# Kernel optimization log

Measured on AMD Instinct MI355X. Metric: run time of the kernel, lower is better.

The kernel has to match this reference:

```python
import jax, jax.numpy as jnp
import numpy as np

N_NODES = 20000
N_EDGES = 200000
D = 64            # node_encoding
H = 4             # num_heads
GRAPH_LAYERS = 2
FLOW_ITERS = 10


def seg_softmax(logits, seg, n):
    # numerically stable softmax over segments (per-row softmax of sparse matrix)
    m = jax.ops.segment_max(logits, seg, num_segments=n)
    e = jnp.exp(logits - m[seg])
    s = jax.ops.segment_sum(e, seg, num_segments=n)
    return e / s[seg]


def setup_inputs() -> dict:
    key = jax.random.key(0)
    ks = jax.random.split(key, 12)
    sc = 1.0 / np.sqrt(D)
    return {
        "node_embeddings": jax.random.normal(ks[0], (N_NODES, D), jnp.float32),
        "demands": jax.random.normal(ks[1], (N_NODES, 1), jnp.float32),
        "edge_row": jax.random.randint(ks[2], (N_EDGES,), 0, N_NODES, jnp.int32),
        "edge_col": jax.random.randint(ks[3], (N_EDGES,), 0, N_NODES, jnp.int32),
        "W_gat": jax.random.normal(ks[4], (H, D, D), jnp.float32) * sc,
        "a_src": jax.random.normal(ks[5], (H, D), jnp.float32) * sc,
        "a_dst": jax.random.normal(ks[6], (H, D), jnp.float32) * sc,
        "Wx": jax.random.normal(ks[7], (D, 3 * D), jnp.float32) * sc,
        "Wh": jax.random.normal(ks[8], (D, 3 * D), jnp.float32) * sc,
        "b_gru": jnp.zeros((3 * D,), jnp.float32),
        "Wd": jax.random.normal(ks[9], (D + 1, 1), jnp.float32) * sc,
        "bd": jnp.zeros((1,), jnp.float32),
    }


def reference(node_embeddings, demands, edge_row, edge_col,
              W_gat, a_src, a_dst, Wx, Wh, b_gru, Wd, bd):
    n = node_embeddings.shape[0]
    h = node_embeddings

    for _ in range(GRAPH_LAYERS):
        # ---- SparseGAT over adjacency edge list ----
        f = jnp.einsum('nd,hde->hne', h, W_gat)          # [H,N,D] per-head features
        s_src = jnp.einsum('hne,he->hn', f, a_src)       # [H,N]
        s_dst = jnp.einsum('hne,he->hn', f, a_dst)       # [H,N]
        logits = jax.nn.leaky_relu(s_src[:, edge_row] + s_dst[:, edge_col], 0.2)  # [H,E]
        alpha = jax.vmap(lambda l: seg_softmax(l, edge_row, n))(logits)           # [H,E]
        msgs = alpha[:, :, None] * f[:, edge_col, :]                              # [H,E,D]
        agg = jax.vmap(lambda m: jax.ops.segment_sum(m, edge_row, num_segments=n))(msgs)  # [H,N,D]
        gat_out = agg.mean(axis=0)                       # average heads -> [N,D]

        # ---- GRU node update (relu candidate activation), state = h ----
        xg = gat_out @ Wx + b_gru                        # [N,3D]
        z = jax.nn.sigmoid(xg[:, :D] + h @ Wh[:, :D])
        r = jax.nn.sigmoid(xg[:, D:2 * D] + h @ Wh[:, D:2 * D])
        hh = jax.nn.relu(xg[:, 2 * D:] + (r * h) @ Wh[:, 2 * D:])
        h = z * h + (1.0 - z) * hh

    # ---- decoder: linear over concat(encoding, demands) ----
    pred_w = jnp.concatenate([h, demands], axis=1) @ Wd + bd   # [N,1]

    # ---- sparse softmax of (adj * pred_weights) per source row ----
    w = seg_softmax(pred_w[edge_row, 0], edge_row, n)          # [E]

    # ---- iterative sparse MCF flow solve ----
    d_pos = jax.nn.relu(demands[:, 0])                         # source injections

    def step(flow, _):
        inflow = d_pos + jax.ops.segment_sum(flow, edge_col, num_segments=n)
        return w * inflow[edge_row], None

    flow, _ = jax.lax.scan(step, jnp.zeros_like(w), None, length=FLOW_ITERS)
    return flow
```

## Files before the change

### kernel.cpp

```cpp
#include <hip/hip_runtime.h>


#define N_NODES 20000
#define N_EDGES 200000
#define FLOW_ITERS 10
#define NBLK 128
#define NTHR 512
#define NTOT (NBLK * NTHR)
#define EPT ((N_EDGES + NTOT - 1) / NTOT)
#define NPB 157
#define CAP 24
#define SLOTS NTOT
#define OFL_MAX 4096
#define NP1 (N_NODES + 1)

__device__ __forceinline__ float ld_coh(const float* p) {
    return __hip_atomic_load(p, __ATOMIC_RELAXED, __HIP_MEMORY_SCOPE_AGENT);
}
__device__ __forceinline__ int ld_coh_i(const int* p) {
    return __hip_atomic_load(p, __ATOMIC_RELAXED, __HIP_MEMORY_SCOPE_AGENT);
}
__device__ __forceinline__ void st_coh(float* p, float v) {
    __hip_atomic_store(p, v, __ATOMIC_RELAXED, __HIP_MEMORY_SCOPE_AGENT);
}
__device__ __forceinline__ void st_coh_i(int* p, int v) {
    __hip_atomic_store(p, v, __ATOMIC_RELAXED, __HIP_MEMORY_SCOPE_AGENT);
}

__device__ __forceinline__ void gbar(int* cnt, int target) {
    __syncthreads();
    if (threadIdx.x == 0) {
        __hip_atomic_fetch_add(cnt, 1, __ATOMIC_RELAXED, __HIP_MEMORY_SCOPE_AGENT);
        while (__hip_atomic_load(cnt, __ATOMIC_RELAXED, __HIP_MEMORY_SCOPE_AGENT) < target)
            __builtin_amdgcn_s_sleep(2);
    }
    __syncthreads();
}

__global__ __launch_bounds__(NTHR)
void mcf_fused(const float* __restrict__ demands,
               const int* __restrict__ edge_row,
               const int* __restrict__ edge_col,
               float* __restrict__ out,
               int* __restrict__ deg,
               int* __restrict__ fill,
               float* __restrict__ V0,
               float* __restrict__ V1b,
               int* __restrict__ pcsc,
               int* __restrict__ ofl_cnt,
               int* __restrict__ ofl_v,
               int* __restrict__ ofl_row,
               int* __restrict__ barcnt)
{
    const int tid = blockIdx.x * NTHR + threadIdx.x;
    int bar = 0;

    int rowr[EPT];
    #pragma unroll
    for (int i = 0; i < EPT; ++i) {
        int e = tid + i * NTOT;
        rowr[i] = N_NODES;
        if (e < N_EDGES) {
            int r = edge_row[e], c = edge_col[e];
            rowr[i] = r;
            __hip_atomic_fetch_add(&deg[r], 1, __ATOMIC_RELAXED, __HIP_MEMORY_SCOPE_AGENT);
            int idx = __hip_atomic_fetch_add(&fill[c], 1,
                                             __ATOMIC_RELAXED, __HIP_MEMORY_SCOPE_AGENT);
            int slot = (c / NPB) * NTHR + (c % NPB);
            if (idx < CAP) {
                st_coh_i(&pcsc[slot * CAP + idx], r);
            } else {
                int o = __hip_atomic_fetch_add(ofl_cnt, 1,
                                               __ATOMIC_RELAXED, __HIP_MEMORY_SCOPE_AGENT);
                if (o < OFL_MAX) { st_coh_i(&ofl_v[o], c); st_coh_i(&ofl_row[o], r); }
            }
        }
    }
    gbar(barcnt, NBLK * (++bar));

    const int tx = threadIdx.x;
    const int v  = blockIdx.x * NPB + tx;
    const bool active = (tx < NPB) && (v < N_NODES);
    float dposv = 0.0f, invd = 0.0f;
    int   cnt = 0, ocnt = 0;
    int   er[CAP];
    if (active) {
        dposv  = fmaxf(demands[v], 0.0f);
        int dv = ld_coh_i(&deg[v]);
        invd   = (dv > 0) ? (1.0f / (float)dv) : 0.0f;
        cnt    = min(ld_coh_i(&fill[v]), CAP);
        ocnt   = ld_coh_i(ofl_cnt);
        const int slot = blockIdx.x * NTHR + tx;
        #pragma unroll
        for (int k = 0; k < CAP; ++k) {
            int r = pcsc[slot * CAP + k];
            er[k] = (k < cnt) ? r : N_NODES;
        }
        st_coh(&V0[v], dposv * invd);
    }
    gbar(barcnt, NBLK * (++bar));

    #pragma unroll 1
    for (int j = 2; j <= FLOW_ITERS; ++j) {
        const float* Vp = (j & 1) ? V1b : V0;
        float*       Vn = (j & 1) ? V0 : V1b;
        if (active) {
            float sk[CAP];
            #pragma unroll
            for (int s = 0; s < CAP; ++s) sk[s] = ld_coh(&Vp[er[s]]);
            float acc = dposv;
            #pragma unroll
            for (int s = 0; s < CAP; ++s) acc += sk[s];
            if (ocnt > 0) {
                for (int o = 0; o < ocnt && o < OFL_MAX; ++o)
                    if (ld_coh_i(&ofl_v[o]) == v)
                        acc += ld_coh(&Vp[ld_coh_i(&ofl_row[o])]);
            }
            st_coh(&Vn[v], acc * invd);
        }
        gbar(barcnt, NBLK * (++bar));
    }

    #pragma unroll
    for (int i = 0; i < EPT; ++i) {
        int e = tid + i * NTOT;
        if (e < N_EDGES) out[e] = ld_coh(&V1b[rowr[i]]);
    }
}

extern "C" void kernel_launch(void* const* d_in, const int* in_sizes, int n_in,
                              void* d_out, int out_size, void* d_ws, size_t ws_size,
                              hipStream_t stream) {
    const float* demands  = (const float*)d_in[1];
    const int*   edge_row = (const int*)d_in[2];
    const int*   edge_col = (const int*)d_in[3];
    float*       out      = (float*)d_out;

    char* ws = (char*)d_ws;
    auto take = [&](size_t bytes) {
        void* p = (void*)ws;
        ws += (bytes + 127) & ~size_t(127);
        return p;
    };
    char* zone0 = ws;
    int*   deg     = (int*)  take(N_NODES * 4);
    int*   fill    = (int*)  take(N_NODES * 4);
    float* V0      = (float*)take(NP1 * 4);
    float* V1b     = (float*)take(NP1 * 4);
    int*   ofl_cnt = (int*)  take(4);
    int*   barcnt  = (int*)  take(4);
    size_t zone0_bytes = (size_t)(ws - zone0);
    int*   pcsc    = (int*)  take((size_t)SLOTS * CAP * 4);
    int*   ofl_v   = (int*)  take(OFL_MAX * 4);
    int*   ofl_row = (int*)  take(OFL_MAX * 4);

    hipMemsetAsync(zone0, 0x00, zone0_bytes, stream);
    mcf_fused<<<NBLK, NTHR, 0, stream>>>(demands, edge_row, edge_col, out,
                                         deg, fill, V0, V1b, pcsc,
                                         ofl_cnt, ofl_v, ofl_row, barcnt);
}
```

Before: 140.6 us.

## Build CSC via per-block LDS histograms and transposed prefix instead of global atomics

Replaces the global atomic degree and fill counters with per-block shared-memory histograms over a contiguous edge chunk. The histograms are written as packed 16-bit counts into per-block tables, and each node then reduces them to a degree and an exclusive prefix of in-edge counts per block. Edges are scattered into the fixed-capacity CSC slots using that prefix plus their local index. This removes heavy contended global atomics, but adds an extra grid barrier, 20000-int LDS zeroing and scanning per block, and 128-way strided reads per node.

```diff
diff --git a/kernel.cpp b/kernel.cpp
--- a/kernel.cpp
+++ b/kernel.cpp
@@ -6,11 +6,13 @@
 #define FLOW_ITERS 10
 #define NBLK 128
 #define NTHR 512
-#define NTOT (NBLK * NTHR)
-#define EPT ((N_EDGES + NTOT - 1) / NTOT)
+#define EPB 1563
+#define EPT ((EPB + NTHR - 1) / NTHR)
 #define NPB 157
 #define CAP 24
-#define SLOTS NTOT
+#define SLOTS (NBLK * NTHR)
+#define NWORD (N_NODES / 2)
+#define NPADV 20224
 #define OFL_MAX 4096
 #define NP1 (N_NODES + 1)
 
@@ -24,6 +26,9 @@
     __hip_atomic_store(p, v, __ATOMIC_RELAXED, __HIP_MEMORY_SCOPE_AGENT);
 }
 __device__ __forceinline__ void st_coh_i(int* p, int v) {
+    __hip_atomic_store(p, v, __ATOMIC_RELAXED, __HIP_MEMORY_SCOPE_AGENT);
+}
+__device__ __forceinline__ void st_coh_u(unsigned* p, unsigned v) {
     __hip_atomic_store(p, v, __ATOMIC_RELAXED, __HIP_MEMORY_SCOPE_AGENT);
 }
 
@@ -35,6 +40,10 @@
             __builtin_amdgcn_s_sleep(2);
     }
     __syncthreads();
+}
+
+__device__ __forceinline__ int half16(int w, int hi) {
+    return hi ? ((w >> 16) & 0xFFFF) : (w & 0xFFFF);
 }
 
 __global__ __launch_bounds__(NTHR)
@@ -42,8 +51,9 @@
                const int* __restrict__ edge_row,
                const int* __restrict__ edge_col,
                float* __restrict__ out,
-               int* __restrict__ deg,
-               int* __restrict__ fill,
+               int* __restrict__ degT,
+               int* __restrict__ inhT,
+               unsigned* __restrict__ pre32,
                float* __restrict__ V0,
                float* __restrict__ V1b,
                int* __restrict__ pcsc,
@@ -52,53 +62,116 @@
                int* __restrict__ ofl_row,
                int* __restrict__ barcnt)
 {
-    const int tid = blockIdx.x * NTHR + threadIdx.x;
+    const int tx = threadIdx.x, bx = blockIdx.x;
     int bar = 0;
 
-    int rowr[EPT];
+    __shared__ int ldsH[N_NODES];
+
+    int rowr[EPT], colr[EPT], lidx[EPT];
+    for (int i = tx; i < N_NODES; i += NTHR) ldsH[i] = 0;
+    __syncthreads();
     #pragma unroll
     for (int i = 0; i < EPT; ++i) {
-        int e = tid + i * NTOT;
-        rowr[i] = N_NODES;
-        if (e < N_EDGES) {
-            int r = edge_row[e], c = edge_col[e];
-            rowr[i] = r;
-            __hip_atomic_fetch_add(&deg[r], 1, __ATOMIC_RELAXED, __HIP_MEMORY_SCOPE_AGENT);
-            int idx = __hip_atomic_fetch_add(&fill[c], 1,
-                                             __ATOMIC_RELAXED, __HIP_MEMORY_SCOPE_AGENT);
-            int slot = (c / NPB) * NTHR + (c % NPB);
-            if (idx < CAP) {
-                st_coh_i(&pcsc[slot * CAP + idx], r);
-            } else {
-                int o = __hip_atomic_fetch_add(ofl_cnt, 1,
-                                               __ATOMIC_RELAXED, __HIP_MEMORY_SCOPE_AGENT);
-                if (o < OFL_MAX) { st_coh_i(&ofl_v[o], c); st_coh_i(&ofl_row[o], r); }
-            }
-        }
-    }
+        int local = i * NTHR + tx, e = bx * EPB + local;
+        rowr[i] = -1;
+        if (local < EPB && e < N_EDGES) {
+            rowr[i] = edge_row[e];
+            colr[i] = edge_col[e];
+            atomicAdd(&ldsH[rowr[i]], 1);
+        }
+    }
+    __syncthreads();
+    for (int wi = tx; wi < NWORD; wi += NTHR)
+        st_coh_i(&degT[bx * NWORD + wi], ldsH[2 * wi] | (ldsH[2 * wi + 1] << 16));
+    __syncthreads();
+
+    for (int i = tx; i < N_NODES; i += NTHR) ldsH[i] = 0;
+    __syncthreads();
+    #pragma unroll
+    for (int i = 0; i < EPT; ++i)
+        if (rowr[i] >= 0) lidx[i] = atomicAdd(&ldsH[colr[i]], 1);
+    __syncthreads();
+    for (int wi = tx; wi < NWORD; wi += NTHR)
+        st_coh_i(&inhT[bx * NWORD + wi], ldsH[2 * wi] | (ldsH[2 * wi + 1] << 16));
     gbar(barcnt, NBLK * (++bar));
 
-    const int tx = threadIdx.x;
-    const int v  = blockIdx.x * NPB + tx;
+    const int v = bx * NPB + tx;
     const bool active = (tx < NPB) && (v < N_NODES);
     float dposv = 0.0f, invd = 0.0f;
     int   cnt = 0, ocnt = 0;
     int   er[CAP];
     if (active) {
-        dposv  = fmaxf(demands[v], 0.0f);
-        int dv = ld_coh_i(&deg[v]);
-        invd   = (dv > 0) ? (1.0f / (float)dv) : 0.0f;
-        cnt    = min(ld_coh_i(&fill[v]), CAP);
-        ocnt   = ld_coh_i(ofl_cnt);
-        const int slot = blockIdx.x * NTHR + tx;
+        const int wv = v >> 1, hv = v & 1;
+        int sdeg = 0;
+        #pragma unroll 1
+        for (int g = 0; g < NBLK / 8; ++g) {
+            int w0 = ld_coh_i(&degT[(g*8+0) * NWORD + wv]);
+            int w1 = ld_coh_i(&degT[(g*8+1) * NWORD + wv]);
+            int w2 = ld_coh_i(&degT[(g*8+2) * NWORD + wv]);
+            int w3 = ld_coh_i(&degT[(g*8+3) * NWORD + wv]);
+            int w4 = ld_coh_i(&degT[(g*8+4) * NWORD + wv]);
+            int w5 = ld_coh_i(&degT[(g*8+5) * NWORD + wv]);
+            int w6 = ld_coh_i(&degT[(g*8+6) * NWORD + wv]);
+            int w7 = ld_coh_i(&degT[(g*8+7) * NWORD + wv]);
+            sdeg += half16(w0,hv)+half16(w1,hv)+half16(w2,hv)+half16(w3,hv)
+                  + half16(w4,hv)+half16(w5,hv)+half16(w6,hv)+half16(w7,hv);
+        }
+        int acc = 0;
+        #pragma unroll 1
+        for (int g = 0; g < NBLK / 8; ++g) {
+            int w[8];
+            #pragma unroll
+            for (int q = 0; q < 8; ++q)
+                w[q] = ld_coh_i(&inhT[(g*8+q) * NWORD + wv]);
+            unsigned pw0 = 0, pw1 = 0;
+            #pragma unroll
+            for (int q = 0; q < 4; ++q) {
+                pw0 |= (unsigned)min(acc, 255) << (8*q);
+                acc += half16(w[q], hv);
+            }
+            #pragma unroll
+            for (int q = 0; q < 4; ++q) {
+                pw1 |= (unsigned)min(acc, 255) << (8*q);
+                acc += half16(w[4+q], hv);
+            }
+            st_coh_u(&pre32[(g*2+0) * NPADV + v], pw0);
+            st_coh_u(&pre32[(g*2+1) * NPADV + v], pw1);
+        }
+        cnt   = min(acc, CAP);
+        dposv = fmaxf(demands[v], 0.0f);
+        invd  = (sdeg > 0) ? (1.0f / (float)sdeg) : 0.0f;
+        st_coh(&V0[v], dposv * invd);
+    }
+    gbar(barcnt, NBLK * (++bar));
+
+    #pragma unroll
+    for (int i = 0; i < EPT; ++i) {
+        if (rowr[i] >= 0) {
+            int c = colr[i];
+            unsigned pw = pre32[(bx >> 2) * NPADV + c];
+            int pre = (pw >> (8 * (bx & 3))) & 0xFF;
+            int gidx = pre + lidx[i];
+            if (gidx < CAP) {
+                int slot = (c / NPB) * NTHR + (c % NPB);
+                st_coh_i(&pcsc[slot * CAP + gidx], rowr[i]);
+            } else {
+                int o = __hip_atomic_fetch_add(ofl_cnt, 1,
+                                               __ATOMIC_RELAXED, __HIP_MEMORY_SCOPE_AGENT);
+                if (o < OFL_MAX) { st_coh_i(&ofl_v[o], c); st_coh_i(&ofl_row[o], rowr[i]); }
+            }
+        }
+    }
+    gbar(barcnt, NBLK * (++bar));
+
+    if (active) {
+        ocnt = ld_coh_i(ofl_cnt);
+        const int slot = bx * NTHR + tx;
         #pragma unroll
         for (int k = 0; k < CAP; ++k) {
             int r = pcsc[slot * CAP + k];
             er[k] = (k < cnt) ? r : N_NODES;
         }
-        st_coh(&V0[v], dposv * invd);
-    }
-    gbar(barcnt, NBLK * (++bar));
+    }
 
     #pragma unroll 1
     for (int j = 2; j <= FLOW_ITERS; ++j) {
@@ -123,8 +196,8 @@
 
     #pragma unroll
     for (int i = 0; i < EPT; ++i) {
-        int e = tid + i * NTOT;
-        if (e < N_EDGES) out[e] = ld_coh(&V1b[rowr[i]]);
+        int local = i * NTHR + tx, e = bx * EPB + local;
+        if (local < EPB && e < N_EDGES) out[e] = ld_coh(&V1b[rowr[i]]);
     }
 }
 
@@ -143,19 +216,20 @@
         return p;
     };
     char* zone0 = ws;
-    int*   deg     = (int*)  take(N_NODES * 4);
-    int*   fill    = (int*)  take(N_NODES * 4);
-    float* V0      = (float*)take(NP1 * 4);
-    float* V1b     = (float*)take(NP1 * 4);
-    int*   ofl_cnt = (int*)  take(4);
-    int*   barcnt  = (int*)  take(4);
+    float*    V0      = (float*)   take(NP1 * 4);
+    float*    V1b     = (float*)   take(NP1 * 4);
+    int*      ofl_cnt = (int*)     take(4);
+    int*      barcnt  = (int*)     take(4);
     size_t zone0_bytes = (size_t)(ws - zone0);
-    int*   pcsc    = (int*)  take((size_t)SLOTS * CAP * 4);
-    int*   ofl_v   = (int*)  take(OFL_MAX * 4);
-    int*   ofl_row = (int*)  take(OFL_MAX * 4);
+    int*      degT    = (int*)     take((size_t)NBLK * NWORD * 4);
+    int*      inhT    = (int*)     take((size_t)NBLK * NWORD * 4);
+    unsigned* pre32   = (unsigned*)take((size_t)32 * NPADV * 4);
+    int*      pcsc    = (int*)     take((size_t)SLOTS * CAP * 4);
+    int*      ofl_v   = (int*)     take(OFL_MAX * 4);
+    int*      ofl_row = (int*)     take(OFL_MAX * 4);
 
     hipMemsetAsync(zone0, 0x00, zone0_bytes, stream);
     mcf_fused<<<NBLK, NTHR, 0, stream>>>(demands, edge_row, edge_col, out,
-                                         deg, fill, V0, V1b, pcsc,
+                                         degT, inhT, pre32, V0, V1b, pcsc,
                                          ofl_cnt, ofl_v, ofl_row, barcnt);
 }
```

Result: slower. 155.8 us (+10.8%).

## Split node gathers across three lanes, vectorize edge loads, shard grid barrier counter

Applied to the files above, without the earlier changes.

Each node's in-edge gather is now split across three threads, each loading 8 slots of a node-major CSC buffer with int4 reads and skipping empty slots, then summed via shared memory. Edge loading and the final output write use int4/float4 vectorized accesses. The grid barrier counter is sharded into 8 padded counters to reduce atomic contention, with pollers summing all shards. This raises thread utilisation and memory parallelism per flow iteration, at the cost of an extra __syncthreads per iteration and a more expensive barrier poll.

```diff
diff --git a/kernel.cpp b/kernel.cpp
--- a/kernel.cpp
+++ b/kernel.cpp
@@ -6,11 +6,10 @@
 #define FLOW_ITERS 10
 #define NBLK 128
 #define NTHR 512
-#define NTOT (NBLK * NTHR)
-#define EPT ((N_EDGES + NTOT - 1) / NTOT)
 #define NPB 157
 #define CAP 24
-#define SLOTS NTOT
+#define NQUAD 50000
+#define QPB 391
 #define OFL_MAX 4096
 #define NP1 (N_NODES + 1)
 
@@ -27,12 +26,21 @@
     __hip_atomic_store(p, v, __ATOMIC_RELAXED, __HIP_MEMORY_SCOPE_AGENT);
 }
 
-__device__ __forceinline__ void gbar(int* cnt, int target) {
+__device__ __forceinline__ void gbar(int* grp, int ord) {
     __syncthreads();
     if (threadIdx.x == 0) {
-        __hip_atomic_fetch_add(cnt, 1, __ATOMIC_RELAXED, __HIP_MEMORY_SCOPE_AGENT);
-        while (__hip_atomic_load(cnt, __ATOMIC_RELAXED, __HIP_MEMORY_SCOPE_AGENT) < target)
-            __builtin_amdgcn_s_sleep(2);
+        __hip_atomic_fetch_add(&grp[(blockIdx.x & 7) * 32], 1,
+                               __ATOMIC_RELAXED, __HIP_MEMORY_SCOPE_AGENT);
+        const int target = NBLK * ord;
+        for (;;) {
+            int s = 0;
+            #pragma unroll
+            for (int g = 0; g < 8; ++g)
+                s += __hip_atomic_load(&grp[g * 32], __ATOMIC_RELAXED,
+                                       __HIP_MEMORY_SCOPE_AGENT);
+            if (s >= target) break;
+            __builtin_amdgcn_s_sleep(1);
+        }
     }
     __syncthreads();
 }
@@ -50,67 +58,73 @@
                int* __restrict__ ofl_cnt,
                int* __restrict__ ofl_v,
                int* __restrict__ ofl_row,
-               int* __restrict__ barcnt)
+               int* __restrict__ grp)
 {
-    const int tid = blockIdx.x * NTHR + threadIdx.x;
+    const int tx = threadIdx.x, bx = blockIdx.x;
     int bar = 0;
 
-    int rowr[EPT];
-    #pragma unroll
-    for (int i = 0; i < EPT; ++i) {
-        int e = tid + i * NTOT;
-        rowr[i] = N_NODES;
-        if (e < N_EDGES) {
-            int r = edge_row[e], c = edge_col[e];
-            rowr[i] = r;
-            __hip_atomic_fetch_add(&deg[r], 1, __ATOMIC_RELAXED, __HIP_MEMORY_SCOPE_AGENT);
-            int idx = __hip_atomic_fetch_add(&fill[c], 1,
+    __shared__ float part[NTHR];
+
+    const int m = bx * QPB + tx;
+    const bool bld = (tx < QPB) && (m < NQUAD);
+    int4 r4 = {0, 0, 0, 0}, c4 = {0, 0, 0, 0};
+    if (bld) {
+        r4 = ((const int4*)edge_row)[m];
+        c4 = ((const int4*)edge_col)[m];
+        int rr[4] = {r4.x, r4.y, r4.z, r4.w};
+        int cc[4] = {c4.x, c4.y, c4.z, c4.w};
+        #pragma unroll
+        for (int i = 0; i < 4; ++i) {
+            __hip_atomic_fetch_add(&deg[rr[i]], 1, __ATOMIC_RELAXED, __HIP_MEMORY_SCOPE_AGENT);
+            int idx = __hip_atomic_fetch_add(&fill[cc[i]], 1,
                                              __ATOMIC_RELAXED, __HIP_MEMORY_SCOPE_AGENT);
-            int slot = (c / NPB) * NTHR + (c % NPB);
             if (idx < CAP) {
-                st_coh_i(&pcsc[slot * CAP + idx], r);
+                st_coh_i(&pcsc[cc[i] * CAP + idx], rr[i]);
             } else {
                 int o = __hip_atomic_fetch_add(ofl_cnt, 1,
                                                __ATOMIC_RELAXED, __HIP_MEMORY_SCOPE_AGENT);
-                if (o < OFL_MAX) { st_coh_i(&ofl_v[o], c); st_coh_i(&ofl_row[o], r); }
+                if (o < OFL_MAX) { st_coh_i(&ofl_v[o], cc[i]); st_coh_i(&ofl_row[o], rr[i]); }
             }
         }
     }
-    gbar(barcnt, NBLK * (++bar));
+    gbar(grp, ++bar);
 
-    const int tx = threadIdx.x;
-    const int v  = blockIdx.x * NPB + tx;
-    const bool active = (tx < NPB) && (v < N_NODES);
+    const int g = tx / 3, q = tx - 3 * g;
+    const int v = bx * NPB + g;
+    const bool active = (g < NPB) && (v < N_NODES);
     float dposv = 0.0f, invd = 0.0f;
     int   cnt = 0, ocnt = 0;
-    int   er[CAP];
+    int   er[8];
     if (active) {
-        dposv  = fmaxf(demands[v], 0.0f);
-        int dv = ld_coh_i(&deg[v]);
-        invd   = (dv > 0) ? (1.0f / (float)dv) : 0.0f;
-        cnt    = min(ld_coh_i(&fill[v]), CAP);
-        ocnt   = ld_coh_i(ofl_cnt);
-        const int slot = blockIdx.x * NTHR + tx;
-        #pragma unroll
-        for (int k = 0; k < CAP; ++k) {
-            int r = pcsc[slot * CAP + k];
-            er[k] = (k < cnt) ? r : N_NODES;
+        cnt = min(ld_coh_i(&fill[v]), CAP);
+        const int4* pb = (const int4*)&pcsc[v * CAP + q * 8];
+        int4 a = pb[0], b = pb[1];
+        er[0]=a.x; er[1]=a.y; er[2]=a.z; er[3]=a.w;
+        er[4]=b.x; er[5]=b.y; er[6]=b.z; er[7]=b.w;
+        if (q == 0) {
+            dposv  = fmaxf(demands[v], 0.0f);
+            int dv = ld_coh_i(&deg[v]);
+            invd   = (dv > 0) ? (1.0f / (float)dv) : 0.0f;
+            ocnt   = ld_coh_i(ofl_cnt);
+            st_coh(&V0[v], dposv * invd);
         }
-        st_coh(&V0[v], dposv * invd);
     }
-    gbar(barcnt, NBLK * (++bar));
+    gbar(grp, ++bar);
 
     #pragma unroll 1
     for (int j = 2; j <= FLOW_ITERS; ++j) {
         const float* Vp = (j & 1) ? V1b : V0;
         float*       Vn = (j & 1) ? V0 : V1b;
         if (active) {
-            float sk[CAP];
+            float p = 0.0f;
             #pragma unroll
-            for (int s = 0; s < CAP; ++s) sk[s] = ld_coh(&Vp[er[s]]);
-            float acc = dposv;
-            #pragma unroll
-            for (int s = 0; s < CAP; ++s) acc += sk[s];
+            for (int s = 0; s < 8; ++s)
+                if (q * 8 + s < cnt) p += ld_coh(&Vp[er[s]]);
+            part[tx] = p;
+        }
+        __syncthreads();
+        if (active && q == 0) {
+            float acc = dposv + part[tx] + part[tx + 1] + part[tx + 2];
             if (ocnt > 0) {
                 for (int o = 0; o < ocnt && o < OFL_MAX; ++o)
                     if (ld_coh_i(&ofl_v[o]) == v)
@@ -118,13 +132,16 @@
             }
             st_coh(&Vn[v], acc * invd);
         }
-        gbar(barcnt, NBLK * (++bar));
+        gbar(grp, ++bar);
     }
 
-    #pragma unroll
-    for (int i = 0; i < EPT; ++i) {
-        int e = tid + i * NTOT;
-        if (e < N_EDGES) out[e] = ld_coh(&V1b[rowr[i]]);
+    if (bld) {
+        float4 o4;
+        o4.x = ld_coh(&V1b[r4.x]);
+        o4.y = ld_coh(&V1b[r4.y]);
+        o4.z = ld_coh(&V1b[r4.z]);
+        o4.w = ld_coh(&V1b[r4.w]);
+        ((float4*)out)[m] = o4;
     }
 }
 
@@ -148,14 +165,14 @@
     float* V0      = (float*)take(NP1 * 4);
     float* V1b     = (float*)take(NP1 * 4);
     int*   ofl_cnt = (int*)  take(4);
-    int*   barcnt  = (int*)  take(4);
+    int*   grp     = (int*)  take(8 * 32 * 4);
     size_t zone0_bytes = (size_t)(ws - zone0);
-    int*   pcsc    = (int*)  take((size_t)SLOTS * CAP * 4);
+    int*   pcsc    = (int*)  take((size_t)N_NODES * CAP * 4);
     int*   ofl_v   = (int*)  take(OFL_MAX * 4);
     int*   ofl_row = (int*)  take(OFL_MAX * 4);
 
     hipMemsetAsync(zone0, 0x00, zone0_bytes, stream);
     mcf_fused<<<NBLK, NTHR, 0, stream>>>(demands, edge_row, edge_col, out,
                                          deg, fill, V0, V1b, pcsc,
-                                         ofl_cnt, ofl_v, ofl_row, barcnt);
+                                         ofl_cnt, ofl_v, ofl_row, grp);
 }
```

Measured after the change: 122.1 us. 13.1% less time.
